# Kernel tuning notes

Measured on AMD Instinct MI355X. Metric: run time of the kernel, lower is better.

The kernel has to match this reference:

```python
import jax, jax.numpy as jnp
import numpy as np

# uniform-measure init scales from torch_model.init_embedding_scale()
MIN_MEAN = (0.0001 + 0.01) / 2.0
MIN_VAR = 0.01 - MIN_MEAN
DELTA_MEAN = (0.9 + 0.999) / 2.0
DELTA_VAR = 0.999 - DELTA_MEAN
EPS = 1e-8

B, V, D = 131072, 100000, 128


def setup_inputs() -> dict:
    key = jax.random.key(0)
    k1, k2, k3, k4 = jax.random.split(key, 4)
    return {
        "t1x": jax.random.randint(k1, (B,), 0, V),
        "t2x": jax.random.randint(k2, (B,), 0, V),
        "min_embed_table": jax.random.normal(k3, (V, D), jnp.float32),
        "delta_embed_table": jax.random.normal(k4, (V, D), jnp.float32),
    }


def _log_vol(mn, mx):
    # log volume of a box under the uniform (unit-cube) measure; [*, D] -> [*]
    return jnp.sum(jnp.log(jnp.maximum(mx - mn, EPS)), axis=-1)


def _box(idx, min_table, delta_table):
    # embedding lookup + affine rescale into the unit cube (get_word_embedding)
    mn = min_table[idx] * MIN_VAR + MIN_MEAN
    dl = delta_table[idx] * DELTA_VAR + DELTA_MEAN
    return mn, mn + dl


def reference(t1x, t2x, min_embed_table, delta_embed_table):
    t1_min, t1_max = _box(t1x, min_embed_table, delta_embed_table)  # [B, D]
    t2_min, t2_max = _box(t2x, min_embed_table, delta_embed_table)

    # unit_cube.calc_join_and_meet
    join_min = jnp.minimum(t1_min, t2_min)
    join_max = jnp.maximum(t1_max, t2_max)
    meet_min = jnp.maximum(t1_min, t2_min)
    meet_max = jnp.minimum(t1_max, t2_max)
    disjoint = jnp.any(meet_max <= meet_min, axis=-1)  # [B] bool

    t1_log = _log_vol(t1_min, t1_max)      # [B]
    t2_log = _log_vol(t2_min, t2_max)
    meet_log = _log_vol(meet_min, meet_max)
    join_log = _log_vol(join_min, join_max)

    # log P(t1 | t2) = log vol(meet) - log vol(t2)
    cond_log = meet_log - t2_log

    # positive pairs: overlap -> -log P(t1|t2); disjoint -> upper-bound surrogate
    # upper bound: P(t1, t2) <= vol(t1)*vol(t2)/vol(join)  =>  P(t1|t2) <= vol(t1)/vol(join)
    pos_overlap = -cond_log
    pos_disjoint = -(t1_log - join_log)

    # negative pairs: overlap -> -log(1 - P(t1|t2)); disjoint -> 0 loss
    neg_overlap = -jnp.log(jnp.maximum(1.0 - jnp.exp(cond_log), EPS))

    # vectorized version of the per-sample python loop over the disjoint flag
    train_pos_prob = jnp.where(disjoint, pos_disjoint, pos_overlap)  # [B]
    train_neg_prob = jnp.where(disjoint, jnp.zeros_like(neg_overlap), neg_overlap)
    return train_pos_prob, train_neg_prob
```

## Files before the change

### kernel.cpp

```cpp
#include <hip/hip_runtime.h>
#include <math.h>


#define EPSF 1e-8f

__global__ __launch_bounds__(256, 4) void box_loss_kernel(
    const int* __restrict__ t1x, const int* __restrict__ t2x,
    const float* __restrict__ min_t, const float* __restrict__ delta_t,
    float* __restrict__ out, int B)
{
    const float MIN_MEAN   = (float)((0.0001 + 0.01) / 2.0);
    const float MIN_VAR    = (float)(0.01 - (0.0001 + 0.01) / 2.0);
    const float DELTA_MEAN = (float)((0.9 + 0.999) / 2.0);
    const float DELTA_VAR  = (float)(0.999 - (0.9 + 0.999) / 2.0);

    int gid  = blockIdx.x * blockDim.x + threadIdx.x;
    int s    = gid >> 3;
    int lane = threadIdx.x & 7;
    if (s >= B) return;

    size_t i1 = (size_t)t1x[s];
    size_t i2 = (size_t)t2x[s];

    const float4* m1 = reinterpret_cast<const float4*>(min_t   + i1 * 128);
    const float4* d1 = reinterpret_cast<const float4*>(delta_t + i1 * 128);
    const float4* m2 = reinterpret_cast<const float4*>(min_t   + i2 * 128);
    const float4* d2 = reinterpret_cast<const float4*>(delta_t + i2 * 128);

    float4 a1[4], b1[4], a2[4], b2[4];
    #pragma unroll
    for (int c = 0; c < 4; ++c) {
        int off = c * 8 + lane;
        a1[c] = m1[off];
        b1[c] = d1[off];
        a2[c] = m2[off];
        b2[c] = d2[off];
    }
#if defined(__has_builtin)
#if __has_builtin(__builtin_amdgcn_sched_barrier)
    __builtin_amdgcn_sched_barrier(0);
#endif
#endif

    float p1 = 1.f, p2 = 1.f, pm = 1.f, pj = 1.f;
    float wmin = 1e30f;

    #pragma unroll
    for (int c = 0; c < 4; ++c) {
        const float* pa1 = reinterpret_cast<const float*>(&a1[c]);
        const float* pb1 = reinterpret_cast<const float*>(&b1[c]);
        const float* pa2 = reinterpret_cast<const float*>(&a2[c]);
        const float* pb2 = reinterpret_cast<const float*>(&b2[c]);
        #pragma unroll
        for (int k = 0; k < 4; ++k) {
            float t1min = fmaf(pa1[k], MIN_VAR, MIN_MEAN);
            float w1    = fmaf(pb1[k], DELTA_VAR, DELTA_MEAN);
            float t2min = fmaf(pa2[k], MIN_VAR, MIN_MEAN);
            float w2    = fmaf(pb2[k], DELTA_VAR, DELTA_MEAN);
            float t1max = t1min + w1;
            float t2max = t2min + w2;

            float mm_ = fmaxf(t1min, t2min);
            float mM_ = fminf(t1max, t2max);
            float jm_ = fminf(t1min, t2min);
            float jM_ = fmaxf(t1max, t2max);

            float wm = mM_ - mm_;
            float wj = jM_ - jm_;

            wmin = fminf(wmin, wm);
            p1 *= w1;
            p2 *= w2;
            pm *= fmaxf(wm, EPSF);
            pj *= wj;
        }
    }

    float l1 = __logf(p1);
    float l2 = __logf(p2);
    float lm = __logf(pm);
    float lj = __logf(pj);

    #pragma unroll
    for (int m = 4; m >= 1; m >>= 1) {
        l1   += __shfl_xor(l1,   m, 64);
        l2   += __shfl_xor(l2,   m, 64);
        lm   += __shfl_xor(lm,   m, 64);
        lj   += __shfl_xor(lj,   m, 64);
        wmin  = fminf(wmin, __shfl_xor(wmin, m, 64));
    }

    if (lane == 0) {
        float cond = lm - l2;
        float pos, neg;
        if (wmin <= 0.f) {
            pos = lj - l1;
            neg = 0.f;
        } else {
            pos = -cond;
            neg = -logf(fmaxf(1.f - expf(cond), EPSF));
        }
        out[s]     = pos;
        out[B + s] = neg;
    }
}

extern "C" void kernel_launch(void* const* d_in, const int* in_sizes, int n_in,
                              void* d_out, int out_size, void* d_ws, size_t ws_size,
                              hipStream_t stream) {
    const int*   t1x     = (const int*)d_in[0];
    const int*   t2x     = (const int*)d_in[1];
    const float* min_t   = (const float*)d_in[2];
    const float* delta_t = (const float*)d_in[3];
    float*       out     = (float*)d_out;

    int B = in_sizes[0];
    int threads = 256;
    int blocks  = (B * 8 + threads - 1) / threads;
    box_loss_kernel<<<blocks, threads, 0, stream>>>(t1x, t2x, min_t, delta_t, out, B);
}
```

Before: 136.4 us.

## Process two samples per thread group to overlap gather loads

Each 8-lane group now handles two samples, one from each half of the batch. All 32 float4 loads for both samples are issued before any computation, which raises memory-level parallelism per thread. The grid is halved and launch bounds drop to 2 blocks per SM to make room for twice the register use. Occupancy falls, but each wavefront keeps twice as many loads in flight.

New measurement: 135.7 us. No clear change (-0.5%).

```diff
diff --git a/kernel.cpp b/kernel.cpp
--- a/kernel.cpp
+++ b/kernel.cpp
@@ -4,59 +4,29 @@
 
 #define EPSF 1e-8f
 
-__global__ __launch_bounds__(256, 4) void box_loss_kernel(
-    const int* __restrict__ t1x, const int* __restrict__ t2x,
-    const float* __restrict__ min_t, const float* __restrict__ delta_t,
-    float* __restrict__ out, int B)
+typedef float f32x4 __attribute__((ext_vector_type(4)));
+
+__device__ __forceinline__ void compute_store(
+    const f32x4 (&A1)[4], const f32x4 (&B1)[4],
+    const f32x4 (&A2)[4], const f32x4 (&B2)[4],
+    float* __restrict__ out, int B, int s, int k)
 {
     const float MIN_MEAN   = (float)((0.0001 + 0.01) / 2.0);
     const float MIN_VAR    = (float)(0.01 - (0.0001 + 0.01) / 2.0);
     const float DELTA_MEAN = (float)((0.9 + 0.999) / 2.0);
     const float DELTA_VAR  = (float)(0.999 - (0.9 + 0.999) / 2.0);
 
-    int gid  = blockIdx.x * blockDim.x + threadIdx.x;
-    int s    = gid >> 3;
-    int lane = threadIdx.x & 7;
-    if (s >= B) return;
-
-    size_t i1 = (size_t)t1x[s];
-    size_t i2 = (size_t)t2x[s];
-
-    const float4* m1 = reinterpret_cast<const float4*>(min_t   + i1 * 128);
-    const float4* d1 = reinterpret_cast<const float4*>(delta_t + i1 * 128);
-    const float4* m2 = reinterpret_cast<const float4*>(min_t   + i2 * 128);
-    const float4* d2 = reinterpret_cast<const float4*>(delta_t + i2 * 128);
-
-    float4 a1[4], b1[4], a2[4], b2[4];
-    #pragma unroll
-    for (int c = 0; c < 4; ++c) {
-        int off = c * 8 + lane;
-        a1[c] = m1[off];
-        b1[c] = d1[off];
-        a2[c] = m2[off];
-        b2[c] = d2[off];
-    }
-#if defined(__has_builtin)
-#if __has_builtin(__builtin_amdgcn_sched_barrier)
-    __builtin_amdgcn_sched_barrier(0);
-#endif
-#endif
-
     float p1 = 1.f, p2 = 1.f, pm = 1.f, pj = 1.f;
     float wmin = 1e30f;
 
     #pragma unroll
     for (int c = 0; c < 4; ++c) {
-        const float* pa1 = reinterpret_cast<const float*>(&a1[c]);
-        const float* pb1 = reinterpret_cast<const float*>(&b1[c]);
-        const float* pa2 = reinterpret_cast<const float*>(&a2[c]);
-        const float* pb2 = reinterpret_cast<const float*>(&b2[c]);
         #pragma unroll
-        for (int k = 0; k < 4; ++k) {
-            float t1min = fmaf(pa1[k], MIN_VAR, MIN_MEAN);
-            float w1    = fmaf(pb1[k], DELTA_VAR, DELTA_MEAN);
-            float t2min = fmaf(pa2[k], MIN_VAR, MIN_MEAN);
-            float w2    = fmaf(pb2[k], DELTA_VAR, DELTA_MEAN);
+        for (int q = 0; q < 4; ++q) {
+            float t1min = fmaf(A1[c][q], MIN_VAR, MIN_MEAN);
+            float w1    = fmaf(B1[c][q], DELTA_VAR, DELTA_MEAN);
+            float t2min = fmaf(A2[c][q], MIN_VAR, MIN_MEAN);
+            float w2    = fmaf(B2[c][q], DELTA_VAR, DELTA_MEAN);
             float t1max = t1min + w1;
             float t2max = t2min + w2;
 
@@ -90,7 +60,7 @@
         wmin  = fminf(wmin, __shfl_xor(wmin, m, 64));
     }
 
-    if (lane == 0) {
+    if (k == 0) {
         float cond = lm - l2;
         float pos, neg;
         if (wmin <= 0.f) {
@@ -105,6 +75,60 @@
     }
 }
 
+__global__ __launch_bounds__(256, 2) void box_loss_pipe2_kernel(
+    const int* __restrict__ t1x, const int* __restrict__ t2x,
+    const float* __restrict__ min_t, const float* __restrict__ delta_t,
+    float* __restrict__ out, int B)
+{
+    const int gid  = blockIdx.x * blockDim.x + threadIdx.x;
+    const int grp  = gid >> 3;
+    const int k    = gid & 7;
+    const int half = (B + 1) >> 1;
+
+    const int sA = grp;
+    const int sB = grp + half;
+    if (sA >= B) return;
+    const bool hasB = (sB < B);
+
+    const size_t i1a = (size_t)t1x[sA];
+    const size_t i2a = (size_t)t2x[sA];
+    const int    sBc = hasB ? sB : sA;
+    const size_t i1b = (size_t)t1x[sBc];
+    const size_t i2b = (size_t)t2x[sBc];
+
+    const f32x4* m1a = reinterpret_cast<const f32x4*>(min_t   + i1a * 128);
+    const f32x4* d1a = reinterpret_cast<const f32x4*>(delta_t + i1a * 128);
+    const f32x4* m2a = reinterpret_cast<const f32x4*>(min_t   + i2a * 128);
+    const f32x4* d2a = reinterpret_cast<const f32x4*>(delta_t + i2a * 128);
+    const f32x4* m1b = reinterpret_cast<const f32x4*>(min_t   + i1b * 128);
+    const f32x4* d1b = reinterpret_cast<const f32x4*>(delta_t + i1b * 128);
+    const f32x4* m2b = reinterpret_cast<const f32x4*>(min_t   + i2b * 128);
+    const f32x4* d2b = reinterpret_cast<const f32x4*>(delta_t + i2b * 128);
+
+    f32x4 a1[4], b1[4], a2[4], b2[4];
+    f32x4 c1[4], e1[4], c2[4], e2[4];
+    #pragma unroll
+    for (int c = 0; c < 4; ++c) {
+        const int off = c * 8 + k;
+        a1[c] = m1a[off];
+        b1[c] = d1a[off];
+        a2[c] = m2a[off];
+        b2[c] = d2a[off];
+    }
+    #pragma unroll
+    for (int c = 0; c < 4; ++c) {
+        const int off = c * 8 + k;
+        c1[c] = m1b[off];
+        e1[c] = d1b[off];
+        c2[c] = m2b[off];
+        e2[c] = d2b[off];
+    }
+
+    compute_store(a1, b1, a2, b2, out, B, sA, k);
+    if (hasB)
+        compute_store(c1, e1, c2, e2, out, B, sB, k);
+}
+
 extern "C" void kernel_launch(void* const* d_in, const int* in_sizes, int n_in,
                               void* d_out, int out_size, void* d_ws, size_t ws_size,
                               hipStream_t stream) {
@@ -115,7 +139,8 @@
     float*       out     = (float*)d_out;
 
     int B = in_sizes[0];
+    int half    = (B + 1) >> 1;
     int threads = 256;
-    int blocks  = (B * 8 + threads - 1) / threads;
-    box_loss_kernel<<<blocks, threads, 0, stream>>>(t1x, t2x, min_t, delta_t, out, B);
+    int blocks  = (half * 8 + threads - 1) / threads;
+    box_loss_pipe2_kernel<<<blocks, threads, 0, stream>>>(t1x, t2x, min_t, delta_t, out, B);
 }
```
